# Kernel tuning notes

Measured on AMD Instinct MI355X. Metric: run time of the kernel, lower is better.

The kernel has to match this reference:

```python
import jax, jax.numpy as jnp
import numpy as np

M, N_GRID, DIM = 32, 32, 128
N_SAMPLES = 100000


def setup_inputs() -> dict:
    key = jax.random.key(0)
    k1, k2 = jax.random.split(key)
    x = jax.random.normal(k1, (N_SAMPLES, DIM), dtype=jnp.float32)
    som_weights = jax.random.normal(k2, (M, N_GRID, DIM), dtype=jnp.float32)
    return {"x": x, "som_weights": som_weights}


def reference(x, som_weights):
    # MiniSom.activation_response([v]) puts a 1 at the best-matching unit
    # (argmin Euclidean distance over the m*n prototype grid), then flattens.
    # Batched equivalent: [N, K] squared distances -> argmin -> one-hot.
    K = som_weights.shape[0] * som_weights.shape[1]
    w = som_weights.reshape(K, -1)                       # [K, dim]
    x_sq = jnp.sum(x * x, axis=1, keepdims=True)         # [N, 1]
    w_sq = jnp.sum(w * w, axis=1)                        # [K]
    # squared Euclidean distance; argmin identical to argmin of true distance
    d2 = x_sq + w_sq[None, :] - 2.0 * (x @ w.T)          # [N, K]
    bmu = jnp.argmin(d2, axis=1)                         # [N]
    return jax.nn.one_hot(bmu, K, dtype=jnp.float32)     # [N, K]
```

## Files before the change

kernel.cpp:

```cpp
#include <hip/hip_runtime.h>


typedef __attribute__((ext_vector_type(8))) short bf16x8;
typedef __attribute__((ext_vector_type(4))) float f32x4;

#define SOM_K 1024
#define SOM_D 128
#define MARGIN 0.02f
#define FLAG_CAP 8192

#define WS_WSQ   64
#define WS_W3    8192
#define WS_FLAGS 532480

static __device__ __forceinline__ unsigned short f2bf(float f) {
    unsigned u = __float_as_uint(f);
    return (unsigned short)((u + 0x7FFFu + ((u >> 16) & 1u)) >> 16);
}
static __device__ __forceinline__ float bf2f(unsigned short h) {
    return __uint_as_float(((unsigned)h) << 16);
}

__global__ __launch_bounds__(256) void som_prep(
    const float* __restrict__ w, unsigned short* __restrict__ w3,
    float* __restrict__ wsq)
{
    __shared__ float ws_[16][SOM_D];
    const int nt = blockIdx.x;
    const int tid = threadIdx.x;

    const float* src = w + (size_t)nt * 16 * SOM_D;
    #pragma unroll
    for (int r = 0; r < 8; ++r) {
        const int e = r * 256 + tid;
        ws_[e >> 7][e & 127] = src[e];
    }
    __syncthreads();

    unsigned short* dst = w3 + (size_t)nt * 4096;
    #pragma unroll
    for (int r = 0; r < 2; ++r) {
        const int G = r * 256 + tid;
        const int s = G >> 6;
        const int l = G & 63;
        const int c = l & 15, q = l >> 4;
        bf16x8 v;
        #pragma unroll
        for (int j = 0; j < 8; ++j) {
            const int kk = 32 * s + 8 * q + j;
            const int d = kk & 127;
            const float f = ws_[c][d];
            const unsigned short h = f2bf(f);
            v[j] = (short)((kk & 128) ? f2bf(f - bf2f(h)) : h);
        }
        *(bf16x8*)(dst + G * 8) = v;
    }

    if (tid < 16) {
        double s = 0.0;
        #pragma unroll 16
        for (int d = 0; d < SOM_D; ++d) {
            double v = (double)ws_[tid][d];
            s += v * v;
        }
        wsq[nt * 16 + tid] = (float)s;
    }
}

__global__ __launch_bounds__(64, 2) void som_main(
    const float* __restrict__ x,
    const unsigned short* __restrict__ w3,
    const float* __restrict__ wsq,
    float* __restrict__ out,
    int* __restrict__ flag_count,
    int* __restrict__ flag_list)
{
    const int lane = threadIdx.x;
    const int c = lane & 15;
    const int q = lane >> 4;
    const int R0 = blockIdx.x * 32;

    bf16x8 ah[2][4], al[2][4];
    #pragma unroll
    for (int g = 0; g < 2; ++g) {
        const float* xp = x + (size_t)(R0 + 16 * g + c) * SOM_D + 8 * q;
        #pragma unroll
        for (int s = 0; s < 4; ++s) {
            float4 v0 = *(const float4*)(xp + 32 * s);
            float4 v1 = *(const float4*)(xp + 32 * s + 4);
            float xv[8] = {v0.x, v0.y, v0.z, v0.w, v1.x, v1.y, v1.z, v1.w};
            bf16x8 hh, ll;
            #pragma unroll
            for (int j = 0; j < 8; ++j) {
                unsigned short h = f2bf(xv[j]);
                hh[j] = (short)h;
                ll[j] = (short)f2bf(xv[j] - bf2f(h));
            }
            ah[g][s] = hh; al[g][s] = ll;
        }
    }

    float best[2][4], sec[2][4];
    int bk[2][4];
    #pragma unroll
    for (int g = 0; g < 2; ++g)
        #pragma unroll
        for (int r = 0; r < 4; ++r) { best[g][r] = 1e30f; sec[g][r] = 1e30f; bk[g][r] = 0; }

    const unsigned short* wbase = w3 + lane * 8;

    #pragma unroll 1
    for (int nt = 0; nt < 64; ++nt) {
        const int n0 = nt * 16;
        const unsigned short* wp = wbase + (size_t)nt * 4096;
        bf16x8 b[8];
        #pragma unroll
        for (int s = 0; s < 8; ++s) b[s] = *(const bf16x8*)(wp + 512 * s);
        const float wq = wsq[n0 + c];

        f32x4 a0 = {0.f, 0.f, 0.f, 0.f}, a1 = {0.f, 0.f, 0.f, 0.f};
        #pragma unroll
        for (int s = 0; s < 4; ++s) {
            a0 = __builtin_amdgcn_mfma_f32_16x16x32_bf16(ah[0][s], b[s], a0, 0, 0, 0);
            a1 = __builtin_amdgcn_mfma_f32_16x16x32_bf16(ah[1][s], b[s], a1, 0, 0, 0);
        }
        #pragma unroll
        for (int s = 0; s < 4; ++s) {
            a0 = __builtin_amdgcn_mfma_f32_16x16x32_bf16(ah[0][s], b[4 + s], a0, 0, 0, 0);
            a1 = __builtin_amdgcn_mfma_f32_16x16x32_bf16(ah[1][s], b[4 + s], a1, 0, 0, 0);
        }
        #pragma unroll
        for (int s = 0; s < 4; ++s) {
            a0 = __builtin_amdgcn_mfma_f32_16x16x32_bf16(al[0][s], b[s], a0, 0, 0, 0);
            a1 = __builtin_amdgcn_mfma_f32_16x16x32_bf16(al[1][s], b[s], a1, 0, 0, 0);
        }

        #pragma unroll
        for (int r = 0; r < 4; ++r) {
            float s0 = wq - 2.f * a0[r];
            if (s0 < best[0][r]) { sec[0][r] = best[0][r]; best[0][r] = s0; bk[0][r] = n0 + c; }
            else if (s0 < sec[0][r]) sec[0][r] = s0;
            float s1 = wq - 2.f * a1[r];
            if (s1 < best[1][r]) { sec[1][r] = best[1][r]; best[1][r] = s1; bk[1][r] = n0 + c; }
            else if (s1 < sec[1][r]) sec[1][r] = s1;
        }
    }

    #pragma unroll
    for (int g = 0; g < 2; ++g) {
        #pragma unroll
        for (int r = 0; r < 4; ++r) {
            float b0v = best[g][r], s0v = sec[g][r];
            int k0 = bk[g][r];
            #pragma unroll
            for (int m = 1; m < 16; m <<= 1) {
                float ob = __shfl_xor(b0v, m);
                float os = __shfl_xor(s0v, m);
                int   ok = __shfl_xor(k0, m);
                if (ob < b0v || (ob == b0v && ok < k0)) {
                    s0v = fminf(b0v, os); b0v = ob; k0 = ok;
                } else {
                    s0v = fminf(s0v, ob);
                }
            }
            best[g][r] = b0v; sec[g][r] = s0v; bk[g][r] = k0;
        }
    }

    if (c == 0) {
        #pragma unroll
        for (int g = 0; g < 2; ++g) {
            #pragma unroll
            for (int r = 0; r < 4; ++r) {
                if (sec[g][r] - best[g][r] < MARGIN) {
                    int i = atomicAdd(flag_count, 1);
                    if (i < FLAG_CAP) flag_list[i] = R0 + g * 16 + 4 * q + r;
                }
            }
        }
    }

    #pragma unroll 1
    for (int rr = 0; rr < 32; ++rr) {
        const int g = rr >> 4, qq = (rr >> 2) & 3, r = rr & 3;
        const int b = __shfl(bk[g][r], qq << 4);
        f32x4* op = (f32x4*)(out + (size_t)(R0 + rr) * SOM_K);
        #pragma unroll
        for (int j = 0; j < 4; ++j) {
            const int e = j * 64 + lane;
            f32x4 v = {0.f, 0.f, 0.f, 0.f};
            if ((b >> 2) == e) v[b & 3] = 1.0f;
            __builtin_nontemporal_store(v, op + e);
        }
    }
}

__global__ __launch_bounds__(1024) void som_pass2(
    const float* __restrict__ x,
    const float* __restrict__ w,
    float* __restrict__ out,
    const int* __restrict__ flag_count,
    const int* __restrict__ flag_list)
{
    __shared__ float xs[SOM_D];
    __shared__ double rbest[16];
    __shared__ int    rk[16];

    const int tid  = threadIdx.x;
    const int lane = tid & 63;
    const int wv   = tid >> 6;
    int cnt = *flag_count;
    if (cnt > FLAG_CAP) cnt = FLAG_CAP;

    for (int i = blockIdx.x; i < cnt; i += gridDim.x) {
        const int row = flag_list[i];
        __syncthreads();
        if (tid < SOM_D) xs[tid] = x[(size_t)row * SOM_D + tid];
        __syncthreads();

        const float* wk = w + (size_t)tid * SOM_D;
        double s0 = 0.0, s1 = 0.0;
        #pragma unroll
        for (int d = 0; d < SOM_D; d += 4) {
            float4 wv4 = *(const float4*)(wk + d);
            double w0 = (double)wv4.x, w1 = (double)wv4.y;
            double w2 = (double)wv4.z, w3 = (double)wv4.w;
            s0 += w0 * (w0 - 2.0 * (double)xs[d])     + w2 * (w2 - 2.0 * (double)xs[d + 2]);
            s1 += w1 * (w1 - 2.0 * (double)xs[d + 1]) + w3 * (w3 - 2.0 * (double)xs[d + 3]);
        }
        double sc = s0 + s1;
        int bk = tid;

        #pragma unroll
        for (int off = 32; off > 0; off >>= 1) {
            double os = __shfl_down(sc, off);
            int    ok = __shfl_down(bk, off);
            if (os < sc || (os == sc && ok < bk)) { sc = os; bk = ok; }
        }
        if (lane == 0) { rbest[wv] = sc; rk[wv] = bk; }
        __syncthreads();

        if (tid == 0) {
            double b = rbest[0]; int k0 = rk[0];
            #pragma unroll
            for (int v = 1; v < 16; ++v) {
                if (rbest[v] < b || (rbest[v] == b && rk[v] < k0)) { b = rbest[v]; k0 = rk[v]; }
            }
            rk[0] = k0;
        }
        __syncthreads();
        const int bmu = rk[0];

        out[(size_t)row * SOM_K + tid] = (tid == bmu) ? 1.0f : 0.0f;
    }
}

extern "C" void kernel_launch(void* const* d_in, const int* in_sizes, int n_in,
                              void* d_out, int out_size, void* d_ws, size_t ws_size,
                              hipStream_t stream) {
    const float* x = (const float*)d_in[0];
    const float* w = (const float*)d_in[1];
    float* out = (float*)d_out;

    char* ws = (char*)d_ws;
    int*            flag_count = (int*)ws;
    float*          wsq        = (float*)(ws + WS_WSQ);
    unsigned short* w3         = (unsigned short*)(ws + WS_W3);
    int*            flag_list  = (int*)(ws + WS_FLAGS);

    (void)hipMemsetAsync(d_ws, 0, 64, stream);

    som_prep<<<64, 256, 0, stream>>>(w, w3, wsq);
    som_main<<<3125, 64, 0, stream>>>(x, w3, wsq, out, flag_count, flag_list);
    som_pass2<<<256, 1024, 0, stream>>>(x, w, out, flag_count, flag_list);
}
```

Measured before the change: 645.0 us.

## Stage SOM weights through double-buffered LDS shared by four waves per block

The main kernel now runs four waves per block, each handling 32 rows. Weight tiles are brought into LDS with global_load_lds in a double-buffered loop, so all four waves read them from shared memory instead of each wave loading the same tiles from global/L2 into registers. This cuts redundant weight traffic and overlaps the next tile's load with the current MFMA work. In exchange it adds a barrier per phase and bounds checks for the partial last block.

```diff
diff --git a/kernel.cpp b/kernel.cpp
--- a/kernel.cpp
+++ b/kernel.cpp
@@ -6,6 +6,7 @@
 
 #define SOM_K 1024
 #define SOM_D 128
+#define SOM_N 100000
 #define MARGIN 0.02f
 #define FLAG_CAP 8192
 
@@ -19,6 +20,12 @@
 }
 static __device__ __forceinline__ float bf2f(unsigned short h) {
     return __uint_as_float(((unsigned)h) << 16);
+}
+
+static __device__ __forceinline__ void gl_lds16(const void* g, void* l) {
+    __builtin_amdgcn_global_load_lds(
+        (const __attribute__((address_space(1))) void*)g,
+        (__attribute__((address_space(3))) void*)l, 16, 0, 0);
 }
 
 __global__ __launch_bounds__(256) void som_prep(
@@ -67,7 +74,7 @@
     }
 }
 
-__global__ __launch_bounds__(64, 2) void som_main(
+__global__ __launch_bounds__(256, 3) void som_main(
     const float* __restrict__ x,
     const unsigned short* __restrict__ w3,
     const float* __restrict__ wsq,
@@ -75,15 +82,28 @@
     int* __restrict__ flag_count,
     int* __restrict__ flag_list)
 {
-    const int lane = threadIdx.x;
+    __shared__ char smem[2][16384];
+
+    const int tid  = threadIdx.x;
+    const int lane = tid & 63;
+    const int wv   = tid >> 6;
     const int c = lane & 15;
     const int q = lane >> 4;
-    const int R0 = blockIdx.x * 32;
+    const int R0 = blockIdx.x * 128 + wv * 32;
+
+    {
+        const char* g = (const char*)w3 + (size_t)wv * 4096 + (size_t)lane * 16;
+        char* l = &smem[0][wv * 4096];
+        #pragma unroll
+        for (int i = 0; i < 4; ++i) gl_lds16(g + i * 1024, l + i * 1024);
+    }
 
     bf16x8 ah[2][4], al[2][4];
     #pragma unroll
     for (int g = 0; g < 2; ++g) {
-        const float* xp = x + (size_t)(R0 + 16 * g + c) * SOM_D + 8 * q;
+        int rbase = R0 + 16 * g + c;
+        if (rbase > SOM_N - 1) rbase = SOM_N - 1;
+        const float* xp = x + (size_t)rbase * SOM_D + 8 * q;
         #pragma unroll
         for (int s = 0; s < 4; ++s) {
             float4 v0 = *(const float4*)(xp + 32 * s);
@@ -107,43 +127,57 @@
         #pragma unroll
         for (int r = 0; r < 4; ++r) { best[g][r] = 1e30f; sec[g][r] = 1e30f; bk[g][r] = 0; }
 
-    const unsigned short* wbase = w3 + lane * 8;
+    __syncthreads();
 
     #pragma unroll 1
-    for (int nt = 0; nt < 64; ++nt) {
-        const int n0 = nt * 16;
-        const unsigned short* wp = wbase + (size_t)nt * 4096;
-        bf16x8 b[8];
-        #pragma unroll
-        for (int s = 0; s < 8; ++s) b[s] = *(const bf16x8*)(wp + 512 * s);
-        const float wq = wsq[n0 + c];
-
-        f32x4 a0 = {0.f, 0.f, 0.f, 0.f}, a1 = {0.f, 0.f, 0.f, 0.f};
-        #pragma unroll
-        for (int s = 0; s < 4; ++s) {
-            a0 = __builtin_amdgcn_mfma_f32_16x16x32_bf16(ah[0][s], b[s], a0, 0, 0, 0);
-            a1 = __builtin_amdgcn_mfma_f32_16x16x32_bf16(ah[1][s], b[s], a1, 0, 0, 0);
-        }
-        #pragma unroll
-        for (int s = 0; s < 4; ++s) {
-            a0 = __builtin_amdgcn_mfma_f32_16x16x32_bf16(ah[0][s], b[4 + s], a0, 0, 0, 0);
-            a1 = __builtin_amdgcn_mfma_f32_16x16x32_bf16(ah[1][s], b[4 + s], a1, 0, 0, 0);
-        }
-        #pragma unroll
-        for (int s = 0; s < 4; ++s) {
-            a0 = __builtin_amdgcn_mfma_f32_16x16x32_bf16(al[0][s], b[s], a0, 0, 0, 0);
-            a1 = __builtin_amdgcn_mfma_f32_16x16x32_bf16(al[1][s], b[s], a1, 0, 0, 0);
-        }
-
-        #pragma unroll
-        for (int r = 0; r < 4; ++r) {
-            float s0 = wq - 2.f * a0[r];
-            if (s0 < best[0][r]) { sec[0][r] = best[0][r]; best[0][r] = s0; bk[0][r] = n0 + c; }
-            else if (s0 < sec[0][r]) sec[0][r] = s0;
-            float s1 = wq - 2.f * a1[r];
-            if (s1 < best[1][r]) { sec[1][r] = best[1][r]; best[1][r] = s1; bk[1][r] = n0 + c; }
-            else if (s1 < sec[1][r]) sec[1][r] = s1;
-        }
+    for (int ph = 0; ph < 32; ++ph) {
+        const int cur = ph & 1;
+        if (ph < 31) {
+            const char* g = (const char*)w3 + (size_t)(ph + 1) * 16384
+                            + (size_t)wv * 4096 + (size_t)lane * 16;
+            char* l = &smem[cur ^ 1][wv * 4096];
+            #pragma unroll
+            for (int i = 0; i < 4; ++i) gl_lds16(g + i * 1024, l + i * 1024);
+        }
+
+        #pragma unroll
+        for (int t = 0; t < 2; ++t) {
+            const int nt = 2 * ph + t;
+            const int n0 = nt * 16;
+            const char* lp = &smem[cur][t * 8192] + lane * 16;
+            bf16x8 b[8];
+            #pragma unroll
+            for (int s = 0; s < 8; ++s) b[s] = *(const bf16x8*)(lp + s * 1024);
+            const float wq = wsq[n0 + c];
+
+            f32x4 a0 = {0.f, 0.f, 0.f, 0.f}, a1 = {0.f, 0.f, 0.f, 0.f};
+            #pragma unroll
+            for (int s = 0; s < 4; ++s) {
+                a0 = __builtin_amdgcn_mfma_f32_16x16x32_bf16(ah[0][s], b[s], a0, 0, 0, 0);
+                a1 = __builtin_amdgcn_mfma_f32_16x16x32_bf16(ah[1][s], b[s], a1, 0, 0, 0);
+            }
+            #pragma unroll
+            for (int s = 0; s < 4; ++s) {
+                a0 = __builtin_amdgcn_mfma_f32_16x16x32_bf16(ah[0][s], b[4 + s], a0, 0, 0, 0);
+                a1 = __builtin_amdgcn_mfma_f32_16x16x32_bf16(ah[1][s], b[4 + s], a1, 0, 0, 0);
+            }
+            #pragma unroll
+            for (int s = 0; s < 4; ++s) {
+                a0 = __builtin_amdgcn_mfma_f32_16x16x32_bf16(al[0][s], b[s], a0, 0, 0, 0);
+                a1 = __builtin_amdgcn_mfma_f32_16x16x32_bf16(al[1][s], b[s], a1, 0, 0, 0);
+            }
+
+            #pragma unroll
+            for (int r = 0; r < 4; ++r) {
+                float s0 = wq - 2.f * a0[r];
+                if (s0 < best[0][r]) { sec[0][r] = best[0][r]; best[0][r] = s0; bk[0][r] = n0 + c; }
+                else if (s0 < sec[0][r]) sec[0][r] = s0;
+                float s1 = wq - 2.f * a1[r];
+                if (s1 < best[1][r]) { sec[1][r] = best[1][r]; best[1][r] = s1; bk[1][r] = n0 + c; }
+                else if (s1 < sec[1][r]) sec[1][r] = s1;
+            }
+        }
+        __syncthreads();
     }
 
     #pragma unroll
@@ -172,9 +206,10 @@
         for (int g = 0; g < 2; ++g) {
             #pragma unroll
             for (int r = 0; r < 4; ++r) {
-                if (sec[g][r] - best[g][r] < MARGIN) {
+                const int row = R0 + g * 16 + 4 * q + r;
+                if (row < SOM_N && sec[g][r] - best[g][r] < MARGIN) {
                     int i = atomicAdd(flag_count, 1);
-                    if (i < FLAG_CAP) flag_list[i] = R0 + g * 16 + 4 * q + r;
+                    if (i < FLAG_CAP) flag_list[i] = row;
                 }
             }
         }
@@ -182,9 +217,11 @@
 
     #pragma unroll 1
     for (int rr = 0; rr < 32; ++rr) {
+        const int row = R0 + rr;
+        if (row >= SOM_N) break;
         const int g = rr >> 4, qq = (rr >> 2) & 3, r = rr & 3;
         const int b = __shfl(bk[g][r], qq << 4);
-        f32x4* op = (f32x4*)(out + (size_t)(R0 + rr) * SOM_K);
+        f32x4* op = (f32x4*)(out + (size_t)row * SOM_K);
         #pragma unroll
         for (int j = 0; j < 4; ++j) {
             const int e = j * 64 + lane;
@@ -271,6 +308,6 @@
     (void)hipMemsetAsync(d_ws, 0, 64, stream);
 
     som_prep<<<64, 256, 0, stream>>>(w, w3, wsq);
-    som_main<<<3125, 64, 0, stream>>>(x, w3, wsq, out, flag_count, flag_list);
+    som_main<<<782, 256, 0, stream>>>(x, w3, wsq, out, flag_count, flag_list);
     som_pass2<<<256, 1024, 0, stream>>>(x, w, out, flag_count, flag_list);
 }
```

Result: slower. 660.1 us (+2.3%).

## Split GEMM/argmin from one-hot writes and double-buffer weight tile loads

Applied to the files above, without the earlier changes.

The main kernel is split in two. One kernel computes the best and second-best distances and the winning index per row and stores a small record. A separate wide kernel writes the one-hot output and flags ambiguous rows. The GEMM loop now double-buffers the weight fragments in registers so the next tile's loads overlap the current tile's MFMAs. The split is meant to stop the long output-store phase from stalling the compute waves, at the cost of an extra launch and a record round trip through memory.

```diff
diff --git a/kernel.cpp b/kernel.cpp
--- a/kernel.cpp
+++ b/kernel.cpp
@@ -6,12 +6,14 @@
 
 #define SOM_K 1024
 #define SOM_D 128
+#define SOM_N 100000
 #define MARGIN 0.02f
 #define FLAG_CAP 8192
 
 #define WS_WSQ   64
 #define WS_W3    8192
 #define WS_FLAGS 532480
+#define WS_REC   565248
 
 static __device__ __forceinline__ unsigned short f2bf(float f) {
     unsigned u = __float_as_uint(f);
@@ -67,13 +69,42 @@
     }
 }
 
-__global__ __launch_bounds__(64, 2) void som_main(
+#define TILE_BODY(B_, NT_)                                                     \
+    {                                                                          \
+        const int n0 = (NT_) * 16;                                             \
+        const float wq = wsq[n0 + c];                                          \
+        f32x4 a0 = {0.f, 0.f, 0.f, 0.f}, a1 = {0.f, 0.f, 0.f, 0.f};            \
+        _Pragma("unroll")                                                      \
+        for (int s = 0; s < 4; ++s) {                             \
+            a0 = __builtin_amdgcn_mfma_f32_16x16x32_bf16(ah[0][s], B_[s], a0, 0, 0, 0); \
+            a1 = __builtin_amdgcn_mfma_f32_16x16x32_bf16(ah[1][s], B_[s], a1, 0, 0, 0); \
+        }                                                                      \
+        _Pragma("unroll")                                                      \
+        for (int s = 0; s < 4; ++s) {                             \
+            a0 = __builtin_amdgcn_mfma_f32_16x16x32_bf16(ah[0][s], B_[4 + s], a0, 0, 0, 0); \
+            a1 = __builtin_amdgcn_mfma_f32_16x16x32_bf16(ah[1][s], B_[4 + s], a1, 0, 0, 0); \
+        }                                                                      \
+        _Pragma("unroll")                                                      \
+        for (int s = 0; s < 4; ++s) {          \
+            a0 = __builtin_amdgcn_mfma_f32_16x16x32_bf16(al[0][s], B_[s], a0, 0, 0, 0); \
+            a1 = __builtin_amdgcn_mfma_f32_16x16x32_bf16(al[1][s], B_[s], a1, 0, 0, 0); \
+        }                                                                      \
+        _Pragma("unroll")                                                      \
+        for (int r = 0; r < 4; ++r) {                                          \
+            float s0 = wq - 2.f * a0[r];                                       \
+            if (s0 < best[0][r]) { sec[0][r] = best[0][r]; best[0][r] = s0; bk[0][r] = n0 + c; } \
+            else if (s0 < sec[0][r]) sec[0][r] = s0;                           \
+            float s1 = wq - 2.f * a1[r];                                       \
+            if (s1 < best[1][r]) { sec[1][r] = best[1][r]; best[1][r] = s1; bk[1][r] = n0 + c; } \
+            else if (s1 < sec[1][r]) sec[1][r] = s1;                           \
+        }                                                                      \
+    }
+
+__global__ __launch_bounds__(64, 2) void som_gemm(
     const float* __restrict__ x,
     const unsigned short* __restrict__ w3,
     const float* __restrict__ wsq,
-    float* __restrict__ out,
-    int* __restrict__ flag_count,
-    int* __restrict__ flag_list)
+    float4* __restrict__ rec)
 {
     const int lane = threadIdx.x;
     const int c = lane & 15;
@@ -109,41 +140,27 @@
 
     const unsigned short* wbase = w3 + lane * 8;
 
+    bf16x8 bA[8], bB[8];
+    #pragma unroll
+    for (int s = 0; s < 8; ++s) bA[s] = *(const bf16x8*)(wbase + 512 * s);
+
     #pragma unroll 1
-    for (int nt = 0; nt < 64; ++nt) {
-        const int n0 = nt * 16;
-        const unsigned short* wp = wbase + (size_t)nt * 4096;
-        bf16x8 b[8];
-        #pragma unroll
-        for (int s = 0; s < 8; ++s) b[s] = *(const bf16x8*)(wp + 512 * s);
-        const float wq = wsq[n0 + c];
-
-        f32x4 a0 = {0.f, 0.f, 0.f, 0.f}, a1 = {0.f, 0.f, 0.f, 0.f};
-        #pragma unroll
-        for (int s = 0; s < 4; ++s) {
-            a0 = __builtin_amdgcn_mfma_f32_16x16x32_bf16(ah[0][s], b[s], a0, 0, 0, 0);
-            a1 = __builtin_amdgcn_mfma_f32_16x16x32_bf16(ah[1][s], b[s], a1, 0, 0, 0);
-        }
-        #pragma unroll
-        for (int s = 0; s < 4; ++s) {
-            a0 = __builtin_amdgcn_mfma_f32_16x16x32_bf16(ah[0][s], b[4 + s], a0, 0, 0, 0);
-            a1 = __builtin_amdgcn_mfma_f32_16x16x32_bf16(ah[1][s], b[4 + s], a1, 0, 0, 0);
-        }
-        #pragma unroll
-        for (int s = 0; s < 4; ++s) {
-            a0 = __builtin_amdgcn_mfma_f32_16x16x32_bf16(al[0][s], b[s], a0, 0, 0, 0);
-            a1 = __builtin_amdgcn_mfma_f32_16x16x32_bf16(al[1][s], b[s], a1, 0, 0, 0);
-        }
-
-        #pragma unroll
-        for (int r = 0; r < 4; ++r) {
-            float s0 = wq - 2.f * a0[r];
-            if (s0 < best[0][r]) { sec[0][r] = best[0][r]; best[0][r] = s0; bk[0][r] = n0 + c; }
-            else if (s0 < sec[0][r]) sec[0][r] = s0;
-            float s1 = wq - 2.f * a1[r];
-            if (s1 < best[1][r]) { sec[1][r] = best[1][r]; best[1][r] = s1; bk[1][r] = n0 + c; }
-            else if (s1 < sec[1][r]) sec[1][r] = s1;
-        }
+    for (int ntp = 0; ntp < 32; ++ntp) {
+        const int ntE = 2 * ntp;
+        const int ntO = ntE + 1;
+        {
+            const unsigned short* wp = wbase + (size_t)ntO * 4096;
+            #pragma unroll
+            for (int s = 0; s < 8; ++s) bB[s] = *(const bf16x8*)(wp + 512 * s);
+        }
+        TILE_BODY(bA, ntE)
+        {
+            const int ntN = (ntp < 31) ? ntE + 2 : 0;
+            const unsigned short* wp = wbase + (size_t)ntN * 4096;
+            #pragma unroll
+            for (int s = 0; s < 8; ++s) bA[s] = *(const bf16x8*)(wp + 512 * s);
+        }
+        TILE_BODY(bB, ntO)
     }
 
     #pragma unroll
@@ -172,26 +189,43 @@
         for (int g = 0; g < 2; ++g) {
             #pragma unroll
             for (int r = 0; r < 4; ++r) {
-                if (sec[g][r] - best[g][r] < MARGIN) {
-                    int i = atomicAdd(flag_count, 1);
-                    if (i < FLAG_CAP) flag_list[i] = R0 + g * 16 + 4 * q + r;
-                }
+                const int row = R0 + g * 16 + 4 * q + r;
+                float4 rv;
+                rv.x = best[g][r];
+                rv.y = sec[g][r];
+                rv.z = __int_as_float(bk[g][r]);
+                rv.w = 0.f;
+                rec[row] = rv;
             }
         }
     }
-
-    #pragma unroll 1
-    for (int rr = 0; rr < 32; ++rr) {
-        const int g = rr >> 4, qq = (rr >> 2) & 3, r = rr & 3;
-        const int b = __shfl(bk[g][r], qq << 4);
-        f32x4* op = (f32x4*)(out + (size_t)(R0 + rr) * SOM_K);
-        #pragma unroll
-        for (int j = 0; j < 4; ++j) {
-            const int e = j * 64 + lane;
-            f32x4 v = {0.f, 0.f, 0.f, 0.f};
-            if ((b >> 2) == e) v[b & 3] = 1.0f;
-            __builtin_nontemporal_store(v, op + e);
-        }
+}
+
+__global__ __launch_bounds__(256) void som_write(
+    const float4* __restrict__ rec,
+    float* __restrict__ out,
+    int* __restrict__ flag_count,
+    int* __restrict__ flag_list)
+{
+    const int lane = threadIdx.x & 63;
+    const int wv   = threadIdx.x >> 6;
+    const int row  = blockIdx.x * 4 + wv;
+
+    const float4 r = rec[row];
+    const int b = __float_as_int(r.z);
+
+    if (lane == 0 && (r.y - r.x < MARGIN)) {
+        int i = atomicAdd(flag_count, 1);
+        if (i < FLAG_CAP) flag_list[i] = row;
+    }
+
+    f32x4* op = (f32x4*)(out + (size_t)row * SOM_K);
+    #pragma unroll
+    for (int j = 0; j < 4; ++j) {
+        const int e = j * 64 + lane;
+        f32x4 v = {0.f, 0.f, 0.f, 0.f};
+        if ((b >> 2) == e) v[b & 3] = 1.0f;
+        __builtin_nontemporal_store(v, op + e);
     }
 }
 
@@ -267,10 +301,12 @@
     float*          wsq        = (float*)(ws + WS_WSQ);
     unsigned short* w3         = (unsigned short*)(ws + WS_W3);
     int*            flag_list  = (int*)(ws + WS_FLAGS);
+    float4*         rec        = (float4*)(ws + WS_REC);
 
     (void)hipMemsetAsync(d_ws, 0, 64, stream);
 
     som_prep<<<64, 256, 0, stream>>>(w, w3, wsq);
-    som_main<<<3125, 64, 0, stream>>>(x, w3, wsq, out, flag_count, flag_list);
+    som_gemm<<<3125, 64, 0, stream>>>(x, w3, wsq, rec);
+    som_write<<<25000, 256, 0, stream>>>(rec, out, flag_count, flag_list);
     som_pass2<<<256, 1024, 0, stream>>>(x, w, out, flag_count, flag_list);
 }
```

After: 640.6 us (median of 2 runs). About the same (-0.7%).
